# Kernel tuning notes

Hardware: AMD Instinct MI355X
Metric: run time of the kernel (lower is better)

Reference implementation:

```python
import jax, jax.numpy as jnp
from jax import lax
import numpy as np

B, T, IN, H = 4096, 200, 79, 10  # batch, seq_len, input_size, hidden_size


def setup_inputs() -> dict:
    key = jax.random.key(0)
    ks = jax.random.split(key, 12)
    f32 = jnp.float32
    return {
        "x": jax.random.normal(ks[0], (B, T, IN), f32),
        # BayesianLSTM reparameterized params: W = mu + softplus(rho) * eps
        "wih_mu": jax.random.normal(ks[1], (IN, 4 * H), f32) * 0.1,
        "wih_rho": jnp.full((IN, 4 * H), -3.0, f32),
        "wih_eps": jax.random.normal(ks[2], (IN, 4 * H), f32),
        "whh_mu": jax.random.normal(ks[3], (H, 4 * H), f32) * 0.1,
        "whh_rho": jnp.full((H, 4 * H), -3.0, f32),
        "whh_eps": jax.random.normal(ks[4], (H, 4 * H), f32),
        "b_mu": jax.random.normal(ks[5], (4 * H,), f32) * 0.1,
        "b_rho": jnp.full((4 * H,), -3.0, f32),
        "b_eps": jax.random.normal(ks[6], (4 * H,), f32),
        # deterministic linear head (10 -> 1)
        "lin_w": jax.random.normal(ks[7], (H, 1), f32) * 0.3,
        "lin_b": jax.random.normal(ks[8], (1,), f32) * 0.1,
    }


def reference(x, wih_mu, wih_rho, wih_eps, whh_mu, whh_rho, whh_eps,
              b_mu, b_rho, b_eps, lin_w, lin_b):
    sp = jax.nn.softplus
    Wih = wih_mu + sp(wih_rho) * wih_eps   # [IN, 4H]
    Whh = whh_mu + sp(whh_rho) * whh_eps   # [H, 4H]
    b = b_mu + sp(b_rho) * b_eps           # [4H]

    # Precompute input projection for all timesteps: [T, B, 4H]
    xg = jnp.einsum('bti,ig->tbg', x, Wih) + b

    h0 = jnp.zeros((x.shape[0], Whh.shape[0]), x.dtype)
    c0 = h0

    def step(carry, g_t):
        h, c = carry
        gates = g_t + h @ Whh
        i, f, g, o = jnp.split(gates, 4, axis=-1)
        i = jax.nn.sigmoid(i)
        f = jax.nn.sigmoid(f)
        g = jnp.tanh(g)
        o = jax.nn.sigmoid(o)
        c = f * c + i * g
        h = o * jnp.tanh(c)
        return (h, c), None

    (hT, _), _ = lax.scan(step, (h0, c0), xg)
    # x_[:, -1, :] == final hidden state hT; then linear head
    return hT @ lin_w + lin_b  # [B, 1]
```

## Files before the change

kernel.cpp:

```cpp
#include <hip/hip_runtime.h>
#include <cstdint>

#define Bsz 4096
#define Tlen 200
#define INs 79
#define Hs 10
#define Gs 40

typedef __attribute__((ext_vector_type(8))) short bf16x8;
typedef __attribute__((ext_vector_type(4))) float f32x4;

__device__ __forceinline__ unsigned short f2bf(float x) {
    unsigned u = __float_as_uint(x);
    return (unsigned short)((u + 0x7FFF + ((u >> 16) & 1)) >> 16);
}

__global__ void prep_kernel(const float* __restrict__ wih_mu, const float* __restrict__ wih_rho, const float* __restrict__ wih_eps,
                            const float* __restrict__ whh_mu, const float* __restrict__ whh_rho, const float* __restrict__ whh_eps,
                            const float* __restrict__ b_mu,   const float* __restrict__ b_rho,   const float* __restrict__ b_eps,
                            float* __restrict__ w) {
    int idx = blockIdx.x * 256 + threadIdx.x;
    if (idx < 4608) {
        int c = idx / 96, k = idx % 96;
        float val = 0.0f;
        if (c < Gs && k < INs) {
            int s = k * Gs + c;
            float r = wih_rho[s];
            float sp = (r > 20.0f) ? r : log1pf(expf(r));
            val = fmaf(sp, wih_eps[s], wih_mu[s]);
        }
        unsigned short h = f2bf(val);
        float back = __uint_as_float((unsigned)h << 16);
        unsigned short l = f2bf(val - back);
        ((unsigned short*)(w + 512))[idx]  = h;
        ((unsigned short*)(w + 2816))[idx] = l;
    } else if (idx < 5008) {
        int m = idx - 4608;
        float r = whh_rho[m];
        float sp = (r > 20.0f) ? r : log1pf(expf(r));
        w[48 + m] = fmaf(sp, whh_eps[m], whh_mu[m]);
    } else if (idx < 5056) {
        int m = idx - 5008;
        float val = 0.0f;
        if (m < Gs) {
            float r = b_rho[m];
            float sp = (r > 20.0f) ? r : log1pf(expf(r));
            val = fmaf(sp, b_eps[m], b_mu[m]);
        }
        w[m] = val;
    }
}

__global__ __launch_bounds__(64, 4) void fused_kernel(
    const float* __restrict__ x, const float* __restrict__ w,
    const float* __restrict__ lin_w, const float* __restrict__ lin_b,
    float* __restrict__ out) {
    __shared__ __align__(16) float sm[1280 + 16 * 42];
    float* xbuf = sm;
    float* gbuf = sm + 1280;

    const int b = blockIdx.x;
    const int lane = threadIdx.x;
    const int jj = lane & 15;
    const int kg8 = (lane >> 4) * 8;

    if (lane < 16) sm[1264 + lane] = 0.0f;

    const unsigned short* Bh = (const unsigned short*)(w + 512);
    const unsigned short* Bl = (const unsigned short*)(w + 2816);

    int pj = (lane & 3) * 10 + (lane >> 2); if (pj > 39) pj = 39;
    const int ty = lane & 3;
    const float sA = (ty == 2) ? -2.0f : -1.0f;
    const float sM = (ty == 2) ?  2.0f :  1.0f;
    const float sC = (ty == 2) ? -1.0f :  0.0f;
    float wcs[Hs];
#pragma unroll
    for (int k = 0; k < Hs; ++k) wcs[k] = w[48 + k * Gs + pj] * sA;
    float bias3[3];
#pragma unroll
    for (int n = 0; n < 3; ++n) bias3[n] = w[n * 16 + jj];

    float hs[Hs];
#pragma unroll
    for (int k = 0; k < Hs; ++k) hs[k] = 0.0f;
    float cc = 0.0f;

    const long xbaseB = (long)b * (Tlen * INs) * 4;
    const long xendB  = (long)Bsz * Tlen * INs * 4 - 16;
    auto* ldsc = (__attribute__((address_space(3))) char*)xbuf;

    auto stage = [&](int t0) {
        long srcB = xbaseB + (long)t0 * INs * 4;
#pragma unroll
        for (int kk = 0; kk < 4; ++kk) {
            long off = srcB + (long)(kk * 64 + lane) * 16;
            if (off > xendB) off = xendB;
            __builtin_amdgcn_global_load_lds(
                (const __attribute__((address_space(1))) void*)((const char*)x + off),
                (__attribute__((address_space(3))) void*)(ldsc + (kk * 64 + lane) * 16), 16, 0, 0);
        }
        if (lane < 60) {
            long off = srcB + (long)(256 + lane) * 16;
            if (off > xendB) off = xendB;
            __builtin_amdgcn_global_load_lds(
                (const __attribute__((address_space(1))) void*)((const char*)x + off),
                (__attribute__((address_space(3))) void*)(ldsc + (256 + lane) * 16), 16, 0, 0);
        }
    };

    stage(0);

    for (int tile = 0; tile < 13; ++tile) {
        const int t0 = tile * 16;
        asm volatile("s_waitcnt vmcnt(0)" ::: "memory");

        float f0[8], f1[8], f2[8];
#pragma unroll
        for (int e = 0; e < 8; ++e) f0[e] = xbuf[jj * INs + kg8 + e];
#pragma unroll
        for (int e = 0; e < 8; ++e) f1[e] = xbuf[jj * INs + 32 + kg8 + e];
#pragma unroll
        for (int e = 0; e < 8; ++e) f2[e] = xbuf[jj * INs + 64 + kg8 + e];
        asm volatile("s_waitcnt lgkmcnt(0)" ::: "memory");
        if (tile < 12) stage(t0 + 16);

        union { unsigned u[4]; bf16x8 v; } Ah[3], Al[3];
        const float* fp[3] = {f0, f1, f2};
#pragma unroll
        for (int ks = 0; ks < 3; ++ks) {
#pragma unroll
            for (int p = 0; p < 4; ++p) {
                float a = fp[ks][2 * p], bb = fp[ks][2 * p + 1];
                unsigned ua = __float_as_uint(a), ub = __float_as_uint(bb);
                Ah[ks].u[p] = __builtin_amdgcn_perm(ub, ua, 0x07060302);
                float ra = a  - __uint_as_float(ua & 0xFFFF0000u);
                float rb = bb - __uint_as_float(ub & 0xFFFF0000u);
                unsigned pk;
                asm("v_cvt_pk_bf16_f32 %0, %1, %2" : "=v"(pk) : "v"(ra), "v"(rb));
                Al[ks].u[p] = pk;
            }
        }

        f32x4 acc[3];
#pragma unroll
        for (int n = 0; n < 3; ++n)
            acc[n] = (f32x4){bias3[n], bias3[n], bias3[n], bias3[n]};
#pragma unroll
        for (int ks = 0; ks < 3; ++ks) {
            const int k0 = ks * 32;
#pragma unroll
            for (int n = 0; n < 3; ++n) {
                int boff = (n * 16 + jj) * 96 + k0 + kg8;
                bf16x8 bh = *(const bf16x8*)(Bh + boff);
                bf16x8 bl = *(const bf16x8*)(Bl + boff);
                acc[n] = __builtin_amdgcn_mfma_f32_16x16x32_bf16(Ah[ks].v, bh, acc[n], 0, 0, 0);
                acc[n] = __builtin_amdgcn_mfma_f32_16x16x32_bf16(Ah[ks].v, bl, acc[n], 0, 0, 0);
                acc[n] = __builtin_amdgcn_mfma_f32_16x16x32_bf16(Al[ks].v, bh, acc[n], 0, 0, 0);
            }
        }

#pragma unroll
        for (int n = 0; n < 3; ++n) {
            if (n == 2 && jj >= 8) continue;
#pragma unroll
            for (int r = 0; r < 4; ++r)
                gbuf[((lane >> 4) * 4 + r) * 42 + n * 16 + jj] = acc[n][r];
        }
        float gv[16];
#pragma unroll
        for (int tt = 0; tt < 16; ++tt) gv[tt] = gbuf[tt * 42 + pj] * sA;

#pragma unroll
        for (int tt = 0; tt < 16; ++tt) {
            if (t0 + tt < Tlen) {
                float acs = gv[tt];
#pragma unroll
                for (int k = 0; k < Hs; ++k) acs = fmaf(hs[k], wcs[k], acs);
                float e  = __expf(acs);
                float sg = __builtin_amdgcn_rcpf(1.0f + e);
                float act = fmaf(sg, sM, sC);
                int ai = __float_as_int(act);
                float a1d = __int_as_float(__builtin_amdgcn_mov_dpp(ai, 0xB1, 0xF, 0xF, true));
                float a2d = __int_as_float(__builtin_amdgcn_mov_dpp(ai, 0x4E, 0xF, 0xF, true));
                float a3d = __int_as_float(__builtin_amdgcn_mov_dpp(ai, 0x1B, 0xF, 0xF, true));
                cc = fmaf(a1d, cc, act * a2d);
                float e2 = __expf(-2.0f * cc);
                float th = fmaf(2.0f, __builtin_amdgcn_rcpf(1.0f + e2), -1.0f);
                float hn = a3d * th;
#pragma unroll
                for (int k = 0; k < Hs; ++k)
                    hs[k] = __int_as_float(__builtin_amdgcn_readlane(__float_as_int(hn), 4 * k));
            }
        }
    }

    if (lane == 0) {
        float o = lin_b[0];
#pragma unroll
        for (int k = 0; k < Hs; ++k) o = fmaf(hs[k], lin_w[k], o);
        out[b] = o;
    }
}

extern "C" void kernel_launch(void* const* d_in, const int* in_sizes, int n_in,
                              void* d_out, int out_size, void* d_ws, size_t ws_size,
                              hipStream_t stream) {
    const float* x = (const float*)d_in[0];
    float* w   = (float*)d_ws;
    float* out = (float*)d_out;

    prep_kernel<<<20, 256, 0, stream>>>(
        (const float*)d_in[1], (const float*)d_in[2], (const float*)d_in[3],
        (const float*)d_in[4], (const float*)d_in[5], (const float*)d_in[6],
        (const float*)d_in[7], (const float*)d_in[8], (const float*)d_in[9], w);

    fused_kernel<<<Bsz, 64, 0, stream>>>(
        x, w, (const float*)d_in[10], (const float*)d_in[11], out);
}
```

Before: 105.8 us.

## Double-buffer x tiles in 8-step chunks and overlap MFMA projection with recurrence

Tiles of x shrink from 16 to 8 timesteps and are double-buffered in LDS. The MFMA input projection for the next chunk is issued before the serial recurrence steps of the current chunk, so matrix work and loads overlap the latency-bound LSTM chain. The recurrent dot product is split into two independent FMA chains to shorten the dependency path, and the scale constants are folded so the tanh exponent no longer needs a multiply. The risk is extra LDS traffic and reliance on implicit ordering of the gbuf write and read within one wavefront, since the result is written for the next chunk while the current one is still being consumed.

New measurement: 200.7 us. 89.7% more time.

```diff
diff --git a/kernel.cpp b/kernel.cpp
--- a/kernel.cpp
+++ b/kernel.cpp
@@ -55,8 +55,7 @@
     const float* __restrict__ x, const float* __restrict__ w,
     const float* __restrict__ lin_w, const float* __restrict__ lin_b,
     float* __restrict__ out) {
-    __shared__ __align__(16) float sm[1280 + 16 * 42];
-    float* xbuf = sm;
+    __shared__ __align__(16) float sm[1280 + 336];
     float* gbuf = sm + 1280;
 
     const int b = blockIdx.x;
@@ -64,16 +63,14 @@
     const int jj = lane & 15;
     const int kg8 = (lane >> 4) * 8;
 
-    if (lane < 16) sm[1264 + lane] = 0.0f;
-
     const unsigned short* Bh = (const unsigned short*)(w + 512);
     const unsigned short* Bl = (const unsigned short*)(w + 2816);
 
     int pj = (lane & 3) * 10 + (lane >> 2); if (pj > 39) pj = 39;
     const int ty = lane & 3;
     const float sA = (ty == 2) ? -2.0f : -1.0f;
-    const float sM = (ty == 2) ?  2.0f :  1.0f;
-    const float sC = (ty == 2) ? -1.0f :  0.0f;
+    const float sM = (ty == 2) ? -4.0f : 1.0f;
+    const float sC = (ty == 2) ?  2.0f : 0.0f;
     float wcs[Hs];
 #pragma unroll
     for (int k = 0; k < Hs; ++k) wcs[k] = w[48 + k * Gs + pj] * sA;
@@ -84,47 +81,36 @@
     float hs[Hs];
 #pragma unroll
     for (int k = 0; k < Hs; ++k) hs[k] = 0.0f;
-    float cc = 0.0f;
+    float C = 0.0f;
 
     const long xbaseB = (long)b * (Tlen * INs) * 4;
-    const long xendB  = (long)Bsz * Tlen * INs * 4 - 16;
-    auto* ldsc = (__attribute__((address_space(3))) char*)xbuf;
-
-    auto stage = [&](int t0) {
+    auto* ldsc = (__attribute__((address_space(3))) char*)sm;
+
+    auto stage = [&](int t0, int buf) {
         long srcB = xbaseB + (long)t0 * INs * 4;
 #pragma unroll
-        for (int kk = 0; kk < 4; ++kk) {
-            long off = srcB + (long)(kk * 64 + lane) * 16;
-            if (off > xendB) off = xendB;
+        for (int kk = 0; kk < 2; ++kk)
             __builtin_amdgcn_global_load_lds(
-                (const __attribute__((address_space(1))) void*)((const char*)x + off),
-                (__attribute__((address_space(3))) void*)(ldsc + (kk * 64 + lane) * 16), 16, 0, 0);
-        }
-        if (lane < 60) {
-            long off = srcB + (long)(256 + lane) * 16;
-            if (off > xendB) off = xendB;
+                (const __attribute__((address_space(1))) void*)((const char*)x + srcB + (kk * 64 + lane) * 16),
+                (__attribute__((address_space(3))) void*)(ldsc + buf * 2560 + (kk * 64 + lane) * 16), 16, 0, 0);
+        if (lane < 30)
             __builtin_amdgcn_global_load_lds(
-                (const __attribute__((address_space(1))) void*)((const char*)x + off),
-                (__attribute__((address_space(3))) void*)(ldsc + (256 + lane) * 16), 16, 0, 0);
-        }
-    };
-
-    stage(0);
-
-    for (int tile = 0; tile < 13; ++tile) {
-        const int t0 = tile * 16;
-        asm volatile("s_waitcnt vmcnt(0)" ::: "memory");
-
+                (const __attribute__((address_space(1))) void*)((const char*)x + srcB + (128 + lane) * 16),
+                (__attribute__((address_space(3))) void*)(ldsc + buf * 2560 + (128 + lane) * 16), 16, 0, 0);
+    };
+
+    auto produce = [&](int buf) {
+        const float* xr = sm + buf * 640 + (jj & 7) * INs;
         float f0[8], f1[8], f2[8];
 #pragma unroll
-        for (int e = 0; e < 8; ++e) f0[e] = xbuf[jj * INs + kg8 + e];
-#pragma unroll
-        for (int e = 0; e < 8; ++e) f1[e] = xbuf[jj * INs + 32 + kg8 + e];
-#pragma unroll
-        for (int e = 0; e < 8; ++e) f2[e] = xbuf[jj * INs + 64 + kg8 + e];
-        asm volatile("s_waitcnt lgkmcnt(0)" ::: "memory");
-        if (tile < 12) stage(t0 + 16);
-
+        for (int e = 0; e < 8; ++e) f0[e] = xr[kg8 + e];
+#pragma unroll
+        for (int e = 0; e < 8; ++e) f1[e] = xr[32 + kg8 + e];
+#pragma unroll
+        for (int e = 0; e < 8; ++e) {
+            float raw = xr[64 + kg8 + e];
+            f2[e] = (kg8 + e < 15) ? raw : 0.0f;
+        }
         union { unsigned u[4]; bf16x8 v; } Ah[3], Al[3];
         const float* fp[3] = {f0, f1, f2};
 #pragma unroll
@@ -141,7 +127,6 @@
                 Al[ks].u[p] = pk;
             }
         }
-
         f32x4 acc[3];
 #pragma unroll
         for (int n = 0; n < 3; ++n)
@@ -159,41 +144,64 @@
                 acc[n] = __builtin_amdgcn_mfma_f32_16x16x32_bf16(Al[ks].v, bh, acc[n], 0, 0, 0);
             }
         }
-
-#pragma unroll
-        for (int n = 0; n < 3; ++n) {
-            if (n == 2 && jj >= 8) continue;
-#pragma unroll
-            for (int r = 0; r < 4; ++r)
-                gbuf[((lane >> 4) * 4 + r) * 42 + n * 16 + jj] = acc[n][r];
-        }
-        float gv[16];
-#pragma unroll
-        for (int tt = 0; tt < 16; ++tt) gv[tt] = gbuf[tt * 42 + pj] * sA;
-
-#pragma unroll
-        for (int tt = 0; tt < 16; ++tt) {
-            if (t0 + tt < Tlen) {
-                float acs = gv[tt];
-#pragma unroll
-                for (int k = 0; k < Hs; ++k) acs = fmaf(hs[k], wcs[k], acs);
-                float e  = __expf(acs);
-                float sg = __builtin_amdgcn_rcpf(1.0f + e);
-                float act = fmaf(sg, sM, sC);
-                int ai = __float_as_int(act);
-                float a1d = __int_as_float(__builtin_amdgcn_mov_dpp(ai, 0xB1, 0xF, 0xF, true));
-                float a2d = __int_as_float(__builtin_amdgcn_mov_dpp(ai, 0x4E, 0xF, 0xF, true));
-                float a3d = __int_as_float(__builtin_amdgcn_mov_dpp(ai, 0x1B, 0xF, 0xF, true));
-                cc = fmaf(a1d, cc, act * a2d);
-                float e2 = __expf(-2.0f * cc);
-                float th = fmaf(2.0f, __builtin_amdgcn_rcpf(1.0f + e2), -1.0f);
-                float hn = a3d * th;
-#pragma unroll
-                for (int k = 0; k < Hs; ++k)
-                    hs[k] = __int_as_float(__builtin_amdgcn_readlane(__float_as_int(hn), 4 * k));
+        if ((lane >> 4) < 2) {
+#pragma unroll
+            for (int n = 0; n < 3; ++n) {
+                if (n == 2 && jj >= 8) continue;
+#pragma unroll
+                for (int r = 0; r < 4; ++r)
+                    gbuf[((lane >> 4) * 4 + r) * 42 + n * 16 + jj] = acc[n][r];
             }
         }
+    };
+
+    float gvp[8];
+    auto loadgv = [&]() {
+#pragma unroll
+        for (int tt = 0; tt < 8; ++tt) gvp[tt] = gbuf[tt * 42 + pj] * sA;
+    };
+
+    auto step = [&](float GV) {
+        float a0 = GV;
+        float a1 = hs[1] * wcs[1];
+        a0 = fmaf(hs[0], wcs[0], a0); a1 = fmaf(hs[3], wcs[3], a1);
+        a0 = fmaf(hs[2], wcs[2], a0); a1 = fmaf(hs[5], wcs[5], a1);
+        a0 = fmaf(hs[4], wcs[4], a0); a1 = fmaf(hs[7], wcs[7], a1);
+        a0 = fmaf(hs[6], wcs[6], a0); a1 = fmaf(hs[9], wcs[9], a1);
+        a0 = fmaf(hs[8], wcs[8], a0);
+        float acs = a0 + a1;
+        float e  = __expf(acs);
+        float sg = __builtin_amdgcn_rcpf(1.0f + e);
+        float act = fmaf(sg, sM, sC);
+        int ai = __float_as_int(act);
+        float a1d = __int_as_float(__builtin_amdgcn_mov_dpp(ai, 0xB1, 0xF, 0xF, true));
+        float a2d = __int_as_float(__builtin_amdgcn_mov_dpp(ai, 0x4E, 0xF, 0xF, true));
+        float a3d = __int_as_float(__builtin_amdgcn_mov_dpp(ai, 0x1B, 0xF, 0xF, true));
+        C = fmaf(a1d, C, act * a2d);
+        float e2 = __expf(C);
+        float th = fmaf(2.0f, __builtin_amdgcn_rcpf(1.0f + e2), -1.0f);
+        float hn = a3d * th;
+#pragma unroll
+        for (int k = 0; k < Hs; ++k)
+            hs[k] = __int_as_float(__builtin_amdgcn_readlane(__float_as_int(hn), 4 * k));
+    };
+
+    stage(0, 0);
+    asm volatile("s_waitcnt vmcnt(0)" ::: "memory");
+    stage(8, 1);
+    produce(0);
+    loadgv();
+
+    for (int i = 1; i <= 24; ++i) {
+        asm volatile("s_waitcnt vmcnt(0)" ::: "memory");
+        if (i < 24) stage((i + 1) * 8, (i + 1) & 1);
+        produce(i & 1);
+#pragma unroll
+        for (int tt = 0; tt < 8; ++tt) step(gvp[tt]);
+        loadgv();
     }
+#pragma unroll
+    for (int tt = 0; tt < 8; ++tt) step(gvp[tt]);
 
     if (lane == 0) {
         float o = lin_b[0];
```

## Fold gate scaling into weights, use exp2, split FMA chain, two waves per block

Applied to the files above, without the earlier changes.

The sign and tanh scaling for the gates moves into the precomputed input weights and bias. The cell state is kept pre-scaled by -2*log2e so each step uses exp2 directly, which removes multiplies from the serial recurrence. The ten-term hidden dot product is split into two interleaved FMA chains to shorten the dependency latency. Each block now runs two waves, one batch element each, to change occupancy and scheduling. Out-of-range tail inputs are zero-masked explicitly, and the rescaling of the cell state adds a small numerical-equivalence risk.

New measurement: 108.9 us. +2.9%, slower.

```diff
diff --git a/kernel.cpp b/kernel.cpp
--- a/kernel.cpp
+++ b/kernel.cpp
@@ -1,11 +1,13 @@
 #include <hip/hip_runtime.h>
 #include <cstdint>
+#include <cmath>
 
 #define Bsz 4096
 #define Tlen 200
 #define INs 79
 #define Hs 10
 #define Gs 40
+#define LOG2E 1.4426950408889634f
 
 typedef __attribute__((ext_vector_type(8))) short bf16x8;
 typedef __attribute__((ext_vector_type(4))) float f32x4;
@@ -28,6 +30,7 @@
             float r = wih_rho[s];
             float sp = (r > 20.0f) ? r : log1pf(expf(r));
             val = fmaf(sp, wih_eps[s], wih_mu[s]);
+            val *= (c >= 20 && c < 30) ? -2.0f : -1.0f;
         }
         unsigned short h = f2bf(val);
         float back = __uint_as_float((unsigned)h << 16);
@@ -46,37 +49,39 @@
             float r = b_rho[m];
             float sp = (r > 20.0f) ? r : log1pf(expf(r));
             val = fmaf(sp, b_eps[m], b_mu[m]);
+            val *= (m >= 20 && m < 30) ? -2.0f : -1.0f;
         }
         w[m] = val;
     }
 }
 
-__global__ __launch_bounds__(64, 4) void fused_kernel(
+__global__ __launch_bounds__(128, 4) void fused_kernel(
     const float* __restrict__ x, const float* __restrict__ w,
     const float* __restrict__ lin_w, const float* __restrict__ lin_b,
     float* __restrict__ out) {
-    __shared__ __align__(16) float sm[1280 + 16 * 42];
-    float* xbuf = sm;
-    float* gbuf = sm + 1280;
-
-    const int b = blockIdx.x;
-    const int lane = threadIdx.x;
+    __shared__ __align__(16) float sm[2 * 1952];
+    const int wv = threadIdx.x >> 6;
+    const int lane = threadIdx.x & 63;
+    float* xbuf = sm + wv * 1952;
+    float* gbuf = xbuf + 1280;
+
+    const int b = blockIdx.x * 2 + wv;
     const int jj = lane & 15;
     const int kg8 = (lane >> 4) * 8;
 
-    if (lane < 16) sm[1264 + lane] = 0.0f;
+    if (lane < 16) xbuf[1264 + lane] = 0.0f;
 
     const unsigned short* Bh = (const unsigned short*)(w + 512);
     const unsigned short* Bl = (const unsigned short*)(w + 2816);
 
     int pj = (lane & 3) * 10 + (lane >> 2); if (pj > 39) pj = 39;
     const int ty = lane & 3;
-    const float sA = (ty == 2) ? -2.0f : -1.0f;
-    const float sM = (ty == 2) ?  2.0f :  1.0f;
-    const float sC = (ty == 2) ? -1.0f :  0.0f;
+    const float sAL = ((ty == 2) ? -2.0f : -1.0f) * LOG2E;
+    const float sM  = (ty == 2) ? (-4.0f * LOG2E) : 1.0f;
+    const float sC  = (ty == 2) ? ( 2.0f * LOG2E) : 0.0f;
     float wcs[Hs];
 #pragma unroll
-    for (int k = 0; k < Hs; ++k) wcs[k] = w[48 + k * Gs + pj] * sA;
+    for (int k = 0; k < Hs; ++k) wcs[k] = w[48 + k * Gs + pj] * sAL;
     float bias3[3];
 #pragma unroll
     for (int n = 0; n < 3; ++n) bias3[n] = w[n * 16 + jj];
@@ -84,7 +89,7 @@
     float hs[Hs];
 #pragma unroll
     for (int k = 0; k < Hs; ++k) hs[k] = 0.0f;
-    float cc = 0.0f;
+    float C = 0.0f;
 
     const long xbaseB = (long)b * (Tlen * INs) * 4;
     const long xendB  = (long)Bsz * Tlen * INs * 4 - 16;
@@ -121,7 +126,10 @@
 #pragma unroll
         for (int e = 0; e < 8; ++e) f1[e] = xbuf[jj * INs + 32 + kg8 + e];
 #pragma unroll
-        for (int e = 0; e < 8; ++e) f2[e] = xbuf[jj * INs + 64 + kg8 + e];
+        for (int e = 0; e < 8; ++e) {
+            float raw = xbuf[jj * INs + 64 + kg8 + e];
+            f2[e] = (kg8 + e < 15) ? raw : 0.0f;
+        }
         asm volatile("s_waitcnt lgkmcnt(0)" ::: "memory");
         if (tile < 12) stage(t0 + 16);
 
@@ -169,23 +177,28 @@
         }
         float gv[16];
 #pragma unroll
-        for (int tt = 0; tt < 16; ++tt) gv[tt] = gbuf[tt * 42 + pj] * sA;
+        for (int tt = 0; tt < 16; ++tt) gv[tt] = gbuf[tt * 42 + pj] * LOG2E;
 
 #pragma unroll
         for (int tt = 0; tt < 16; ++tt) {
             if (t0 + tt < Tlen) {
-                float acs = gv[tt];
-#pragma unroll
-                for (int k = 0; k < Hs; ++k) acs = fmaf(hs[k], wcs[k], acs);
-                float e  = __expf(acs);
+                float a0 = gv[tt];
+                float a1 = hs[1] * wcs[1];
+                a0 = fmaf(hs[0], wcs[0], a0); a1 = fmaf(hs[3], wcs[3], a1);
+                a0 = fmaf(hs[2], wcs[2], a0); a1 = fmaf(hs[5], wcs[5], a1);
+                a0 = fmaf(hs[4], wcs[4], a0); a1 = fmaf(hs[7], wcs[7], a1);
+                a0 = fmaf(hs[6], wcs[6], a0); a1 = fmaf(hs[9], wcs[9], a1);
+                a0 = fmaf(hs[8], wcs[8], a0);
+                float acs = a0 + a1;
+                float e  = exp2f(acs);
                 float sg = __builtin_amdgcn_rcpf(1.0f + e);
                 float act = fmaf(sg, sM, sC);
                 int ai = __float_as_int(act);
                 float a1d = __int_as_float(__builtin_amdgcn_mov_dpp(ai, 0xB1, 0xF, 0xF, true));
                 float a2d = __int_as_float(__builtin_amdgcn_mov_dpp(ai, 0x4E, 0xF, 0xF, true));
                 float a3d = __int_as_float(__builtin_amdgcn_mov_dpp(ai, 0x1B, 0xF, 0xF, true));
-                cc = fmaf(a1d, cc, act * a2d);
-                float e2 = __expf(-2.0f * cc);
+                C = fmaf(a1d, C, act * a2d);
+                float e2 = exp2f(C);
                 float th = fmaf(2.0f, __builtin_amdgcn_rcpf(1.0f + e2), -1.0f);
                 float hn = a3d * th;
 #pragma unroll
@@ -215,6 +228,6 @@
         (const float*)d_in[4], (const float*)d_in[5], (const float*)d_in[6],
         (const float*)d_in[7], (const float*)d_in[8], (const float*)d_in[9], w);
 
-    fused_kernel<<<Bsz, 64, 0, stream>>>(
+    fused_kernel<<<Bsz / 2, 128, 0, stream>>>(
         x, w, (const float*)d_in[10], (const float*)d_in[11], out);
 }
```
